# Kernel optimization log

Hardware: AMD Instinct MI355X
Metric: run time of the kernel (lower is better)

## Reference

```python
import jax, jax.numpy as jnp
import numpy as np

RADIUS = 8
EPS = 1e-4


def box_sum(mat, r):
    """Sliding (2r+1)x(2r+1) box sum with border truncation, via double cumsum.
    Operates on the last two axes; mat: [..., H, W]."""
    H, W = mat.shape[-2], mat.shape[-1]
    cs = jnp.cumsum(mat, axis=-2)
    d = jnp.concatenate([
        cs[..., r:2 * r + 1, :],                                   # rows [0, r]
        cs[..., 2 * r + 1:, :] - cs[..., :H - 2 * r - 1, :],       # rows [r+1, H-r)
        cs[..., -1:, :] - cs[..., H - 2 * r - 1:H - r - 1, :],     # rows [H-r, H)
    ], axis=-2)
    cs = jnp.cumsum(d, axis=-1)
    out = jnp.concatenate([
        cs[..., :, r:2 * r + 1],
        cs[..., :, 2 * r + 1:] - cs[..., :, :W - 2 * r - 1],
        cs[..., :, -1:] - cs[..., :, W - 2 * r - 1:W - r - 1],
    ], axis=-1)
    return out


def setup_inputs() -> dict:
    key = jax.random.key(0)
    k1, k2 = jax.random.split(key)
    shape = (1, 3, 4096, 4096)
    i = jax.random.uniform(k1, shape, dtype=jnp.float32)
    p = jax.random.uniform(k2, shape, dtype=jnp.float32)
    return {"i": i, "p": p}


def reference(i, p):
    r, eps = RADIUS, EPS
    H, W = i.shape[-2], i.shape[-1]
    # per-pixel window pixel count (border-truncated)
    N = box_sum(jnp.ones((H, W), dtype=i.dtype), r)  # [H, W], broadcasts over (1, C)
    mean_i = box_sum(i, r) / N
    mean_p = box_sum(p, r) / N
    mean_pi = box_sum(p * i, r) / N
    mean_ii = box_sum(i * i, r) / N
    cov_ip = mean_pi - mean_p * mean_i
    cov_ii = mean_ii - mean_i * mean_i
    a = cov_ip / (cov_ii + eps)
    b = mean_p - a * mean_i
    q = jnp.clip(a * i + b, 0.0, 1.0)
    return q
```

## Files before the change

kernel.cpp:

```cpp
#include <hip/hip_runtime.h>


typedef float v2f __attribute__((ext_vector_type(2)));

#define HH   4096
#define WW   4096
#define CC   3
#define RAD  8
#define LOG2W 12
#define OUTC 112
#define ROWS 35
#define CS   37
#define RS   118
#define TOTALW (CC*CS*RS)
#define WPB  4
#define EPS  1e-4f

__device__ __forceinline__ void scan4(float si, float sp, float spi, float sii,
                                      float& a, float& b, float& c, float& d) {
    asm("v_mov_b32 %0, %4\n\t"
        "v_mov_b32 %1, %5\n\t"
        "v_mov_b32 %2, %6\n\t"
        "v_mov_b32 %3, %7\n\t"
        "v_add_f32_dpp %0, %0, %0 row_shr:1 row_mask:0xf bank_mask:0xf bound_ctrl:0\n\t"
        "v_add_f32_dpp %1, %1, %1 row_shr:1 row_mask:0xf bank_mask:0xf bound_ctrl:0\n\t"
        "v_add_f32_dpp %2, %2, %2 row_shr:1 row_mask:0xf bank_mask:0xf bound_ctrl:0\n\t"
        "v_add_f32_dpp %3, %3, %3 row_shr:1 row_mask:0xf bank_mask:0xf bound_ctrl:0\n\t"
        "v_add_f32_dpp %0, %0, %0 row_shr:2 row_mask:0xf bank_mask:0xf bound_ctrl:0\n\t"
        "v_add_f32_dpp %1, %1, %1 row_shr:2 row_mask:0xf bank_mask:0xf bound_ctrl:0\n\t"
        "v_add_f32_dpp %2, %2, %2 row_shr:2 row_mask:0xf bank_mask:0xf bound_ctrl:0\n\t"
        "v_add_f32_dpp %3, %3, %3 row_shr:2 row_mask:0xf bank_mask:0xf bound_ctrl:0\n\t"
        "v_add_f32_dpp %0, %0, %0 row_shr:4 row_mask:0xf bank_mask:0xf bound_ctrl:0\n\t"
        "v_add_f32_dpp %1, %1, %1 row_shr:4 row_mask:0xf bank_mask:0xf bound_ctrl:0\n\t"
        "v_add_f32_dpp %2, %2, %2 row_shr:4 row_mask:0xf bank_mask:0xf bound_ctrl:0\n\t"
        "v_add_f32_dpp %3, %3, %3 row_shr:4 row_mask:0xf bank_mask:0xf bound_ctrl:0\n\t"
        "v_add_f32_dpp %0, %0, %0 row_shr:8 row_mask:0xf bank_mask:0xf bound_ctrl:0\n\t"
        "v_add_f32_dpp %1, %1, %1 row_shr:8 row_mask:0xf bank_mask:0xf bound_ctrl:0\n\t"
        "v_add_f32_dpp %2, %2, %2 row_shr:8 row_mask:0xf bank_mask:0xf bound_ctrl:0\n\t"
        "v_add_f32_dpp %3, %3, %3 row_shr:8 row_mask:0xf bank_mask:0xf bound_ctrl:0\n\t"
        "v_add_f32_dpp %0, %0, %0 row_bcast:15 row_mask:0xa bank_mask:0xf\n\t"
        "v_add_f32_dpp %1, %1, %1 row_bcast:15 row_mask:0xa bank_mask:0xf\n\t"
        "v_add_f32_dpp %2, %2, %2 row_bcast:15 row_mask:0xa bank_mask:0xf\n\t"
        "v_add_f32_dpp %3, %3, %3 row_bcast:15 row_mask:0xa bank_mask:0xf\n\t"
        "v_add_f32_dpp %0, %0, %0 row_bcast:31 row_mask:0xc bank_mask:0xf\n\t"
        "v_add_f32_dpp %1, %1, %1 row_bcast:31 row_mask:0xc bank_mask:0xf\n\t"
        "v_add_f32_dpp %2, %2, %2 row_bcast:31 row_mask:0xc bank_mask:0xf\n\t"
        "v_add_f32_dpp %3, %3, %3 row_bcast:31 row_mask:0xc bank_mask:0xf"
        : "=&v"(a), "=&v"(b), "=&v"(c), "=&v"(d)
        : "v"(si), "v"(sp), "v"(spi), "v"(sii));
}

__device__ __forceinline__ float bper(int addr, float x) {
    return __int_as_float(__builtin_amdgcn_ds_bpermute(addr, __float_as_int(x)));
}

__global__ __launch_bounds__(256, 4)
void gf_stream_kernel(const float* __restrict__ gi,
                      const float* __restrict__ gp,
                      float* __restrict__ gq) {
    const int lane = threadIdx.x & 63;
    const int wid  = __builtin_amdgcn_readfirstlane(blockIdx.x * WPB + (threadIdx.x >> 6));
    if (wid >= TOTALW) return;

    const int c   = wid / (CS * RS);
    const int rm  = wid - c * (CS * RS);
    const int rs  = rm / CS;
    const int cs  = rm - rs * CS;
    const int xb  = cs * OUTC - RAD;
    const int y0  = rs * ROWS;

    const size_t plane = (size_t)HH << LOG2W;
    const float* Ic = gi + (size_t)c * plane;
    const float* Pc = gp + (size_t)c * plane;
    float*       Qc = gq + (size_t)c * plane;

    const int  gx0 = xb + 2 * lane;
    const bool pv  = (gx0 >= 0) && (gx0 < WW);
    const int  gxc = min(max(gx0, 0), WW - 2);
    const bool outok = (lane >= 4) && (lane < 60) && pv;

    const int   adn = ((lane + 4) & 63) << 2;
    const int   au5 = ((lane - 5) & 63) << 2;
    const int   au4 = ((lane - 4) & 63) << 2;
    const float m5  = (lane >= 5) ? -1.0f : 0.0f;
    const float m4  = (lane >= 4) ? -1.0f : 0.0f;

    const int gx1 = gx0 + 1;
    const int nx0 = min(gx0 + RAD, WW - 1) - max(gx0 - RAD, 0) + 1;
    const int nx1 = min(gx1 + RAD, WW - 1) - max(gx1 - RAD, 0) + 1;
    v2f invnx;
    invnx.x = __builtin_amdgcn_rcpf((float)max(nx0, 1));
    invnx.y = __builtin_amdgcn_rcpf((float)max(nx1, 1));

    const v2f zero = {0.f, 0.f};
    v2f bi[17], bp[17];
    v2f vsi = zero, vsp = zero, vspi = zero, vsii = zero;

#pragma unroll
    for (int k = 0; k < 17; ++k) {
        int yy = y0 - RAD + k;
        v2f a = zero, b = zero;
        if (yy >= 0 && yy < HH) {
            const float* rI = Ic + ((size_t)(unsigned)yy << LOG2W);
            const float* rP = Pc + ((size_t)(unsigned)yy << LOG2W);
            v2f av = *reinterpret_cast<const v2f*>(rI + gxc);
            v2f bv = *reinterpret_cast<const v2f*>(rP + gxc);
            a = pv ? av : zero;
            b = pv ? bv : zero;
        }
        bi[k] = a; bp[k] = b;
        vsi += a; vsp += b;
        vspi = __builtin_elementwise_fma(a, b, vspi);
        vsii = __builtin_elementwise_fma(a, a, vsii);
    }

    v2f pfa = zero, pfb = zero;
    {
        int py = y0 + RAD + 1;
        if (py < HH) {
            const float* rI = Ic + ((size_t)(unsigned)py << LOG2W);
            const float* rP = Pc + ((size_t)(unsigned)py << LOG2W);
            pfa = *reinterpret_cast<const v2f*>(rI + gxc);
            pfb = *reinterpret_cast<const v2f*>(rP + gxc);
        }
    }

    auto emit = [&](int y, v2f icur) {
        float psi  = vsi.x  + vsi.y;
        float psp  = vsp.x  + vsp.y;
        float pspi = vspi.x + vspi.y;
        float psii = vsii.x + vsii.y;
        float Pi_, Pp_, Ppi_, Pii_;
        scan4(psi, psp, pspi, psii, Pi_, Pp_, Ppi_, Pii_);
        float Qi_  = Pi_  - vsi.y;
        float Qp_  = Pp_  - vsp.y;
        float Qpi_ = Ppi_ - vspi.y;
        float Qii_ = Pii_ - vsii.y;

        auto taps = [&](float P_, float Q_) -> v2f {
            float qdn = bper(adn, Q_);
            float pdn = bper(adn, P_);
            float pu5 = bper(au5, P_);
            float qu4 = bper(au4, Q_);
            v2f w;
            w.x = fmaf(m5, pu5, qdn);
            w.y = fmaf(m4, qu4, pdn);
            return w;
        };
        v2f wi  = taps(Pi_,  Qi_);
        v2f wp  = taps(Pp_,  Qp_);
        v2f wpi = taps(Ppi_, Qpi_);
        v2f wii = taps(Pii_, Qii_);

        int   ny  = min(y + RAD, HH - 1) - max(y - RAD, 0) + 1;
        float iny = __builtin_amdgcn_rcpf((float)ny);
        v2f invN  = invnx * iny;
        v2f mi  = wi  * invN;
        v2f mp  = wp  * invN;
        v2f mpi = wpi * invN;
        v2f mii = wii * invN;
        v2f cip = __builtin_elementwise_fma(-mp, mi, mpi);
        v2f cii = __builtin_elementwise_fma(-mi, mi, mii);
        v2f den = cii + EPS;
        v2f ra;
        ra.x = __builtin_amdgcn_rcpf(den.x);
        ra.y = __builtin_amdgcn_rcpf(den.y);
        v2f aa = cip * ra;
        v2f bb = __builtin_elementwise_fma(-aa, mi, mp);
        v2f q  = __builtin_elementwise_fma(aa, icur, bb);
        q = __builtin_elementwise_min(__builtin_elementwise_max(q, zero), (v2f){1.f, 1.f});
        if (outok) {
            float* Qrow = Qc + ((size_t)(unsigned)y << LOG2W);
            *reinterpret_cast<v2f*>(Qrow + gx0) = q;
        }
    };

    emit(y0, bi[8]);

    int y = y0;
#pragma unroll 1
    for (int o = 0; o < 2; ++o) {
#pragma unroll
        for (int u = 0; u < 17; ++u) {
            ++y;
            v2f a0 = bi[u], b0 = bp[u];
            vsi -= a0; vsp -= b0;
            vspi = __builtin_elementwise_fma(-a0, b0, vspi);
            vsii = __builtin_elementwise_fma(-a0, a0, vsii);

            v2f na = pv ? pfa : zero;
            v2f nb = pv ? pfb : zero;
            bi[u] = na; bp[u] = nb;
            vsi += na; vsp += nb;
            vspi = __builtin_elementwise_fma(na, nb, vspi);
            vsii = __builtin_elementwise_fma(na, na, vsii);

            int py = y + RAD + 1;
            if (py < HH) {
                const float* rI = Ic + ((size_t)(unsigned)py << LOG2W);
                const float* rP = Pc + ((size_t)(unsigned)py << LOG2W);
                pfa = *reinterpret_cast<const v2f*>(rI + gxc);
                pfb = *reinterpret_cast<const v2f*>(rP + gxc);
            } else { pfa = zero; pfb = zero; }

            if (y < HH)
                emit(y, bi[(u + 9) % 17]);
        }
    }
}

extern "C" void kernel_launch(void* const* d_in, const int* in_sizes, int n_in,
                              void* d_out, int out_size, void* d_ws, size_t ws_size,
                              hipStream_t stream) {
    const float* gi = (const float*)d_in[0];
    const float* gp = (const float*)d_in[1];
    float* gq = (float*)d_out;
    const int blocks = (TOTALW + WPB - 1) / WPB;
    gf_stream_kernel<<<blocks, 256, 0, stream>>>(gi, gp, gq);
}
```

Baseline: 512.9 us.

## Drop register ring buffer, reload evicted rows from cache, raise occupancy

The 17-row register ring buffers are gone. The rows leaving the window and the centre row are now reloaded from global memory (expected to hit cache) each step, alongside the incoming row. This frees many VGPRs, so launch bounds rise to 6 waves per SIMD. Rows per wave shrink from 35 to 24 to give more waves. The cost is three times the global loads per output row and more redundant halo reads from the shorter strips.

```diff
diff --git a/kernel.cpp b/kernel.cpp
--- a/kernel.cpp
+++ b/kernel.cpp
@@ -9,9 +9,9 @@
 #define RAD  8
 #define LOG2W 12
 #define OUTC 112
-#define ROWS 35
+#define ROWS 24
 #define CS   37
-#define RS   118
+#define RS   171
 #define TOTALW (CC*CS*RS)
 #define WPB  4
 #define EPS  1e-4f
@@ -54,7 +54,7 @@
     return __int_as_float(__builtin_amdgcn_ds_bpermute(addr, __float_as_int(x)));
 }
 
-__global__ __launch_bounds__(256, 4)
+__global__ __launch_bounds__(256, 6)
 void gf_stream_kernel(const float* __restrict__ gi,
                       const float* __restrict__ gp,
                       float* __restrict__ gq) {
@@ -93,8 +93,8 @@
     invnx.y = __builtin_amdgcn_rcpf((float)max(nx1, 1));
 
     const v2f zero = {0.f, 0.f};
-    v2f bi[17], bp[17];
     v2f vsi = zero, vsp = zero, vspi = zero, vsii = zero;
+    v2f cicur = zero;
 
 #pragma unroll
     for (int k = 0; k < 17; ++k) {
@@ -108,22 +108,13 @@
             a = pv ? av : zero;
             b = pv ? bv : zero;
         }
-        bi[k] = a; bp[k] = b;
+        if (k == RAD) cicur = a;
         vsi += a; vsp += b;
         vspi = __builtin_elementwise_fma(a, b, vspi);
         vsii = __builtin_elementwise_fma(a, a, vsii);
     }
 
-    v2f pfa = zero, pfb = zero;
-    {
-        int py = y0 + RAD + 1;
-        if (py < HH) {
-            const float* rI = Ic + ((size_t)(unsigned)py << LOG2W);
-            const float* rP = Pc + ((size_t)(unsigned)py << LOG2W);
-            pfa = *reinterpret_cast<const v2f*>(rI + gxc);
-            pfb = *reinterpret_cast<const v2f*>(rP + gxc);
-        }
-    }
+    v2f pf_oa = zero, pf_ob = zero, pf_fa = zero, pf_fb = zero, pf_ci = zero;
 
     auto emit = [&](int y, v2f icur) {
         float psi  = vsi.x  + vsi.y;
@@ -175,37 +166,49 @@
         }
     };
 
-    emit(y0, bi[8]);
-
     int y = y0;
 #pragma unroll 1
-    for (int o = 0; o < 2; ++o) {
-#pragma unroll
-        for (int u = 0; u < 17; ++u) {
-            ++y;
-            v2f a0 = bi[u], b0 = bp[u];
+    for (int t = 0; t < ROWS; ++t, ++y) {
+        if (y >= HH) break;
+
+        if (t) {
+            v2f a0 = pv ? pf_oa : zero;
+            v2f b0 = pv ? pf_ob : zero;
             vsi -= a0; vsp -= b0;
             vspi = __builtin_elementwise_fma(-a0, b0, vspi);
             vsii = __builtin_elementwise_fma(-a0, a0, vsii);
-
-            v2f na = pv ? pfa : zero;
-            v2f nb = pv ? pfb : zero;
-            bi[u] = na; bp[u] = nb;
+            v2f na = pv ? pf_fa : zero;
+            v2f nb = pv ? pf_fb : zero;
             vsi += na; vsp += nb;
             vspi = __builtin_elementwise_fma(na, nb, vspi);
             vsii = __builtin_elementwise_fma(na, na, vsii);
-
-            int py = y + RAD + 1;
-            if (py < HH) {
-                const float* rI = Ic + ((size_t)(unsigned)py << LOG2W);
-                const float* rP = Pc + ((size_t)(unsigned)py << LOG2W);
-                pfa = *reinterpret_cast<const v2f*>(rI + gxc);
-                pfb = *reinterpret_cast<const v2f*>(rP + gxc);
-            } else { pfa = zero; pfb = zero; }
-
-            if (y < HH)
-                emit(y, bi[(u + 9) % 17]);
-        }
+            cicur = pv ? pf_ci : zero;
+        }
+
+        {
+            int yn = y + 1;
+            pf_oa = zero; pf_ob = zero; pf_fa = zero; pf_fb = zero;
+            if (yn < HH) {
+                const float* rC = Ic + ((size_t)(unsigned)yn << LOG2W);
+                pf_ci = *reinterpret_cast<const v2f*>(rC + gxc);
+                int ye = yn - (RAD + 1);
+                if (ye >= 0) {
+                    const float* rI = Ic + ((size_t)(unsigned)ye << LOG2W);
+                    const float* rP = Pc + ((size_t)(unsigned)ye << LOG2W);
+                    pf_oa = *reinterpret_cast<const v2f*>(rI + gxc);
+                    pf_ob = *reinterpret_cast<const v2f*>(rP + gxc);
+                }
+                int yf = yn + RAD;
+                if (yf < HH) {
+                    const float* rI = Ic + ((size_t)(unsigned)yf << LOG2W);
+                    const float* rP = Pc + ((size_t)(unsigned)yf << LOG2W);
+                    pf_fa = *reinterpret_cast<const v2f*>(rI + gxc);
+                    pf_fb = *reinterpret_cast<const v2f*>(rP + gxc);
+                }
+            }
+        }
+
+        emit(y, cicur);
     }
 }
 
```

Result: slower. 557.6 us (+8.7%).
